# Kernel optimization log

Hardware: AMD Instinct MI355X
Metric: run time of the kernel (lower is better)

The kernel has to match this reference:

```python
import jax, jax.numpy as jnp
import numpy as np

B, S, T, D, H, FF = 4, 96, 96, 512, 8, 2048
DK = D // H
EPS = 1e-5
NEG_SLOPE = 0.01  # LeakyReLU default


def setup_inputs() -> dict:
    key = jax.random.key(0)
    ks = jax.random.split(key, 8)
    w = lambda k, shape: jax.random.normal(k, shape, jnp.float32) * 0.02
    return {
        "x": jax.random.normal(ks[0], (B, S, T, D), jnp.float32),
        "mask_bias": jax.random.uniform(ks[1], (B, S, T), jnp.float32),
        "t_w": w(ks[2], (4, D, D)), "t_b": jnp.zeros((4, D), jnp.float32),
        "s_w": w(ks[3], (4, D, D)), "s_b": jnp.zeros((4, D), jnp.float32),
        "fc_w1": w(ks[4], (D, FF)), "fc_b1": jnp.zeros((FF,), jnp.float32),
        "fc_w2": w(ks[5], (FF, D)), "fc_b2": jnp.zeros((D,), jnp.float32),
        "ln1_g": jnp.ones((D,), jnp.float32), "ln1_b": jnp.zeros((D,), jnp.float32),
        "ln2_g": jnp.ones((D,), jnp.float32), "ln2_b": jnp.zeros((D,), jnp.float32),
    }


def _ln(y, g, b):
    m = y.mean(-1, keepdims=True)
    v = ((y - m) ** 2).mean(-1, keepdims=True)
    return (y - m) / jnp.sqrt(v + EPS) * g + b


def _split_heads(y):
    # (B,S,T,D) -> (B,H,S,T,DK)
    b, s, t, _ = y.shape
    return y.reshape(b, s, t, H, DK).transpose(0, 3, 1, 2, 4)


def _mha(x, w, b, mask_bias, time_axis):
    q = _split_heads(x @ w[0] + b[0])
    k = _split_heads(x @ w[1] + b[1])
    v = _split_heads(x @ w[2] + b[2])
    scale = 1.0 / np.sqrt(DK)
    if time_axis:
        # attention over time axis T: scores (B,H,S,T,T)
        p = jax.nn.softmax(jnp.einsum('bhstd,bhsud->bhstu', q, k) * scale, axis=-1)
        p = p * mask_bias[:, None, :, :, None]            # post-softmax mask
        o = jnp.einsum('bhstu,bhsud->bhstd', p, v)
    else:
        # attention over space axis S: scores (B,H,T,S,S)
        p = jax.nn.softmax(jnp.einsum('bhstd,bhutd->bhtsu', q, k) * scale, axis=-1)
        p = p * mask_bias.transpose(0, 2, 1)[:, None, :, :, None]
        o = jnp.einsum('bhtsu,bhutd->bhstd', p, v)
    o = o.transpose(0, 2, 3, 1, 4).reshape(x.shape)
    return o @ w[3] + b[3]


def reference(x, mask_bias, t_w, t_b, s_w, s_b, fc_w1, fc_b1, fc_w2, fc_b2,
              ln1_g, ln1_b, ln2_g, ln2_b):
    tt = _mha(x, t_w, t_b, mask_bias, True)
    ss = _mha(tt, s_w, s_b, mask_bias, False)
    x1 = _ln(x + ss, ln1_g, ln1_b)
    h = x1 @ fc_w1 + fc_b1
    h = jnp.where(h >= 0, h, NEG_SLOPE * h)
    ff = h @ fc_w2 + fc_b2
    return _ln(x1 + ff, ln2_g, ln2_b)
```

## Files before the change

### kernel.cpp

```cpp
#include <hip/hip_runtime.h>
#include <hip/hip_bf16.h>

#define B_ 4
#define S_ 96
#define T_ 96
#define D_ 512
#define H_ 8
#define FF_ 2048
#define NROWS (B_*S_*T_)
#define EPS_ 1e-5f
#define NEG_ 0.01f
#define DD_ (512*512)

typedef unsigned short u16;
typedef __attribute__((ext_vector_type(8))) short bf16x8;
typedef __attribute__((ext_vector_type(4))) float f32x4;
typedef __attribute__((address_space(1))) const unsigned glb_u32;
typedef __attribute__((address_space(3))) unsigned lds_u32;

__device__ __forceinline__ float bf(u16 u) { return __uint_as_float(((unsigned)u) << 16); }
__device__ __forceinline__ u16 f2bf(float f) {
    __hip_bfloat16 h = __float2bfloat16(f);
    return *reinterpret_cast<u16*>(&h);
}
__device__ __forceinline__ float blo(unsigned v) { return __uint_as_float(v << 16); }
__device__ __forceinline__ float bhi(unsigned v) { return __uint_as_float(v & 0xffff0000u); }

__device__ __forceinline__ float cvt_ld(float x) { return x; }
__device__ __forceinline__ float cvt_ld(u16 x)  { return bf(x); }
__device__ __forceinline__ void cvt_st(float* p, float v) { *p = v; }
__device__ __forceinline__ void cvt_st(u16* p, float v)   { *p = f2bf(v); }

__device__ __forceinline__ void load8(const float* p, float* y) {
    float4 a = *(const float4*)p, b = *(const float4*)(p + 4);
    y[0]=a.x; y[1]=a.y; y[2]=a.z; y[3]=a.w; y[4]=b.x; y[5]=b.y; y[6]=b.z; y[7]=b.w;
}
__device__ __forceinline__ void load8(const u16* p, float* y) {
    uint4 u = *(const uint4*)p;
    y[0]=blo(u.x); y[1]=bhi(u.x); y[2]=blo(u.y); y[3]=bhi(u.y);
    y[4]=blo(u.z); y[5]=bhi(u.z); y[6]=blo(u.w); y[7]=bhi(u.w);
}
__device__ __forceinline__ void store8(float* p, const float* y) {
    *(float4*)p       = make_float4(y[0], y[1], y[2], y[3]);
    *(float4*)(p + 4) = make_float4(y[4], y[5], y[6], y[7]);
}
__device__ __forceinline__ void store8(u16* p, const float* y) {
    ushort4 a, b;
    a.x = f2bf(y[0]); a.y = f2bf(y[1]); a.z = f2bf(y[2]); a.w = f2bf(y[3]);
    b.x = f2bf(y[4]); b.y = f2bf(y[5]); b.z = f2bf(y[6]); b.w = f2bf(y[7]);
    *(ushort4*)p = a; *(ushort4*)(p + 4) = b;
}

__global__ __launch_bounds__(256)
void cvt_f32_bf16(const float* __restrict__ in, u16* __restrict__ out)
{
    const size_t i = ((size_t)blockIdx.x * 256 + threadIdx.x) * 8;
    float y[8];
    load8(in + i, y);
    store8(out + i, y);
}

__global__ __launch_bounds__(256)
void tconv(const float* __restrict__ in, u16* __restrict__ out, int R, int C)
{
    __shared__ float t[32][33];
    const int c0 = blockIdx.x * 32, r0 = blockIdx.y * 32;
    const int tr = threadIdx.x >> 3, c4 = (threadIdx.x & 7) * 4;
    float4 v = *(const float4*)(in + (size_t)(r0 + tr) * C + c0 + c4);
    t[tr][c4] = v.x; t[tr][c4 + 1] = v.y; t[tr][c4 + 2] = v.z; t[tr][c4 + 3] = v.w;
    __syncthreads();
    const int oc = tr, r4 = c4;
    ushort4 u;
    u.x = f2bf(t[r4 + 0][oc]); u.y = f2bf(t[r4 + 1][oc]);
    u.z = f2bf(t[r4 + 2][oc]); u.w = f2bf(t[r4 + 3][oc]);
    *(ushort4*)(out + (size_t)(c0 + oc) * R + r0 + r4) = u;
}

__global__ __launch_bounds__(256)
void tconv8(const float* __restrict__ t_w, const float* __restrict__ s_w,
            u16* __restrict__ out)
{
    __shared__ float t[32][33];
    const int z = blockIdx.z;
    const float* in = (z < 4) ? (t_w + (size_t)z * DD_) : (s_w + (size_t)(z - 4) * DD_);
    u16* o = out + (size_t)z * DD_;
    const int c0 = blockIdx.x * 32, r0 = blockIdx.y * 32;
    const int tr = threadIdx.x >> 3, c4 = (threadIdx.x & 7) * 4;
    float4 v = *(const float4*)(in + (size_t)(r0 + tr) * 512 + c0 + c4);
    t[tr][c4] = v.x; t[tr][c4 + 1] = v.y; t[tr][c4 + 2] = v.z; t[tr][c4 + 3] = v.w;
    __syncthreads();
    const int oc = tr, r4 = c4;
    ushort4 u;
    u.x = f2bf(t[r4 + 0][oc]); u.y = f2bf(t[r4 + 1][oc]);
    u.z = f2bf(t[r4 + 2][oc]); u.w = f2bf(t[r4 + 3][oc]);
    *(ushort4*)(o + (size_t)(c0 + oc) * 512 + r0 + r4) = u;
}

#define GEMM_PRE()                                                              \
    const int tid = threadIdx.x;                                                \
    const int w = tid >> 6, l = tid & 63;                                       \
    const int wr = w >> 1, wc = w & 1;                                          \
    const unsigned gx = gridDim.x;                                              \
    const unsigned nwg = gx * gridDim.y;                                        \
    unsigned f = blockIdx.y * gx + blockIdx.x;                                  \
    f = (f & 7) * (nwg >> 3) + (f >> 3);                                        \
    const int lrow = l >> 3;                                                    \
    const int swz8 = (((l & 7) ^ lrow) << 3);                                   \
    const int fr16 = l & 15;                                                    \
    const int kq = l >> 4;

#define GEMM_COMPUTE()                                                          \
    _Pragma("unroll")                                                           \
    for (int kk = 0; kk < 2; ++kk) {                                            \
        const int sw = ((((kk << 2) | kq)) ^ (fr16 & 7)) << 3;                  \
        bf16x8 af[4], bfr[4];                                                   \
        _Pragma("unroll")                                                       \
        for (int i = 0; i < 4; ++i)                                             \
            af[i] = *(bf16x8*)&As[(wr * 64 + i * 16 + fr16) * 64 + sw];         \
        _Pragma("unroll")                                                       \
        for (int j = 0; j < 4; ++j)                                             \
            bfr[j] = *(bf16x8*)&Bs[(wc * 64 + j * 16 + fr16) * 64 + sw];        \
        _Pragma("unroll")                                                       \
        for (int i = 0; i < 4; ++i)                                             \
            _Pragma("unroll")                                                   \
            for (int j = 0; j < 4; ++j)                                         \
                acc[i][j] = __builtin_amdgcn_mfma_f32_16x16x32_bf16(af[i], bfr[j], acc[i][j], 0, 0, 0); \
    }

template<int ACT, bool ACC, typename TC>
__global__ __launch_bounds__(256)
void gemm2(const u16* __restrict__ A, const u16* __restrict__ WT,
           const float* __restrict__ bias, TC* __restrict__ C,
           int K, int lda, int ldwt, int ldc)
{
    __shared__ u16 As[128 * 64];
    __shared__ u16 Bs[128 * 64];
    GEMM_PRE();
    const int row0 = (int)(f / gx) * 128, col0 = (int)(f % gx) * 128;
    f32x4 acc[4][4] = {};

    for (int kt = 0; kt < K; kt += 64) {
#pragma unroll
        for (int j = 0; j < 4; ++j) {
            const int line = w * 32 + j * 8;
            const u16* asrc = A  + (size_t)(row0 + line + lrow) * lda  + kt + swz8;
            const u16* bsrc = WT + (size_t)(col0 + line + lrow) * ldwt + kt + swz8;
            __builtin_amdgcn_global_load_lds((glb_u32*)asrc, (lds_u32*)&As[line * 64], 16, 0, 0);
            __builtin_amdgcn_global_load_lds((glb_u32*)bsrc, (lds_u32*)&Bs[line * 64], 16, 0, 0);
        }
        __syncthreads();
        GEMM_COMPUTE();
        __syncthreads();
    }
    const int crow = kq * 4;
#pragma unroll
    for (int i = 0; i < 4; ++i)
#pragma unroll
        for (int j = 0; j < 4; ++j) {
            const int col = col0 + wc * 64 + j * 16 + fr16;
            const float bv = ACC ? 0.f : bias[col];
#pragma unroll
            for (int e = 0; e < 4; ++e) {
                const size_t r = (size_t)(row0 + wr * 64 + i * 16 + crow + e);
                TC* cp = &C[r * (size_t)ldc + col];
                float v = acc[i][j][e] + bv;
                if (ACC) v += cvt_ld(*cp);
                if (ACT == 1) v = (v >= 0.f) ? v : NEG_ * v;
                cvt_st(cp, v);
            }
        }
}

template<int ACT, typename TC>
__global__ __launch_bounds__(512)
void gemm3(const u16* __restrict__ A, const u16* __restrict__ WT,
           const float* __restrict__ bias,
           TC* __restrict__ p0, TC* __restrict__ p1, TC* __restrict__ p2,
           int K, int lda, int ldwt, int ldc, int pgshift)
{
    __shared__ u16 lds[65536];
    const int tid = threadIdx.x;
    const int w = tid >> 6, l = tid & 63;
    const int wr = w >> 2, wc = w & 3;
    const unsigned gx = gridDim.x;
    const unsigned nwg = gx * gridDim.y;
    unsigned f = blockIdx.y * gx + blockIdx.x;
    f = (f & 7) * (nwg >> 3) + (f >> 3);
    const int row0 = (int)(f / gx) * 256, colg0 = (int)(f % gx) * 256;
    const int lrow = l >> 3;
    const int swz8 = (((l & 7) ^ lrow) << 3);
    const int fr16 = l & 15;
    const int kq = l >> 4;

    f32x4 acc[8][4] = {};
    const int NT = K >> 6;

    auto stage = [&](int buf, int kt) {
        u16* Ad = lds + buf * 16384;
        u16* Bd = lds + 32768 + buf * 16384;
#pragma unroll
        for (int j = 0; j < 4; ++j) {
            const int lineb = j * 64 + w * 8;
            const int srow = lineb + lrow;
            const u16* asrc = A  + (size_t)(row0  + srow) * lda  + kt + swz8;
            const u16* bsrc = WT + (size_t)(colg0 + srow) * ldwt + kt + swz8;
            __builtin_amdgcn_global_load_lds((glb_u32*)asrc, (lds_u32*)&Ad[lineb * 64], 16, 0, 0);
            __builtin_amdgcn_global_load_lds((glb_u32*)bsrc, (lds_u32*)&Bd[lineb * 64], 16, 0, 0);
        }
    };

    stage(0, 0);
    for (int t = 0; t < NT; ++t) {
        const int cur = t & 1;
        if (t + 1 < NT) {
            stage(cur ^ 1, (t + 1) << 6);
            asm volatile("s_waitcnt vmcnt(8)" ::: "memory");
        } else {
            asm volatile("s_waitcnt vmcnt(0)" ::: "memory");
        }
        __builtin_amdgcn_s_barrier();
        const u16* Ab = lds + cur * 16384;
        const u16* Bb = lds + 32768 + cur * 16384;
        bf16x8 bq[4];
#pragma unroll
        for (int p = 0; p < 4; ++p) {
            const int kk = p >> 1, ih = p & 1;
            const int sw = ((((kk << 2) | kq)) ^ (fr16 & 7)) << 3;
            if (ih == 0) {
#pragma unroll
                for (int j = 0; j < 4; ++j)
                    bq[j] = *(bf16x8*)&Bb[(wc * 64 + j * 16 + fr16) * 64 + sw];
            }
            bf16x8 af[4];
#pragma unroll
            for (int i = 0; i < 4; ++i)
                af[i] = *(bf16x8*)&Ab[(wr * 128 + (ih * 4 + i) * 16 + fr16) * 64 + sw];
            __builtin_amdgcn_s_barrier();
            __builtin_amdgcn_s_setprio(1);
#pragma unroll
            for (int i = 0; i < 4; ++i)
#pragma unroll
                for (int j = 0; j < 4; ++j)
                    acc[ih * 4 + i][j] = __builtin_amdgcn_mfma_f32_16x16x32_bf16(
                        af[i], bq[j], acc[ih * 4 + i][j], 0, 0, 0);
            __builtin_amdgcn_s_setprio(0);
        }
    }
    const int crow = kq * 4;
#pragma unroll
    for (int i = 0; i < 8; ++i)
#pragma unroll
        for (int j = 0; j < 4; ++j) {
            const int colg = colg0 + wc * 64 + j * 16 + fr16;
            TC* Cb = (((unsigned)colg >> pgshift) == 0) ? p0
                   : (((unsigned)colg >> pgshift) == 1) ? p1 : p2;
            const int col = colg & ((1 << pgshift) - 1);
            const float bv = bias[colg];
#pragma unroll
            for (int e = 0; e < 4; ++e) {
                const size_t r = (size_t)(row0 + wr * 128 + i * 16 + crow + e);
                float v = acc[i][j][e] + bv;
                if (ACT == 1) v = (v >= 0.f) ? v : NEG_ * v;
                cvt_st(&Cb[r * (size_t)ldc + col], v);
            }
        }
}

__global__ __launch_bounds__(384)
void attn_mfma(const u16* __restrict__ q, const u16* __restrict__ kbuf,
               const u16* __restrict__ vbuf, const float* __restrict__ mask,
               u16* __restrict__ out, int time_axis)
{
    __shared__ __align__(16) u16 Ks[96][72];
    __shared__ __align__(16) u16 VT[64][104];
    __shared__ __align__(16) u16 Ps[96][104];
    const int g = blockIdx.x;
    const int h = g & 7;
    const int bs = g >> 3;
    const int b = bs / 96, st = bs % 96;
    const size_t base   = time_axis ? ((size_t)(b * 96 + st) * 96) : ((size_t)b * 9216 + st);
    const size_t stride = time_axis ? 1 : 96;
    const int tid = threadIdx.x;
    const int w = tid / 64, l = tid & 63;
    const int fr = l & 15, fk = (l >> 4) * 8;

    for (int task = tid; task < 96 * 8; task += 384) {
        const int r = task >> 3, c = task & 7;
        *(uint4*)&Ks[r][c * 8] =
            *(const uint4*)(kbuf + (base + (size_t)r * stride) * 512 + h * 64 + c * 8);
    }
    for (int task = tid; task < 96 * 8; task += 384) {
        const int r = task >> 3, c = task & 7;
        uint4 dv = *(const uint4*)(vbuf + (base + (size_t)r * stride) * 512 + h * 64 + c * 8);
        const u16* e = (const u16*)&dv;
#pragma unroll
        for (int j = 0; j < 8; ++j) VT[c * 8 + j][r] = e[j];
    }
    const u16* qp = q + (base + (size_t)(16 * w + fr) * stride) * 512 + h * 64;
    bf16x8 aq0 = *(const bf16x8*)(qp + fk);
    bf16x8 aq1 = *(const bf16x8*)(qp + 32 + fk);
    __syncthreads();

    f32x4 s[6] = {};
#pragma unroll
    for (int fc = 0; fc < 6; ++fc) {
        bf16x8 b0 = *(const bf16x8*)&Ks[fc * 16 + fr][fk];
        bf16x8 b1 = *(const bf16x8*)&Ks[fc * 16 + fr][32 + fk];
        s[fc] = __builtin_amdgcn_mfma_f32_16x16x32_bf16(aq0, b0, s[fc], 0, 0, 0);
        s[fc] = __builtin_amdgcn_mfma_f32_16x16x32_bf16(aq1, b1, s[fc], 0, 0, 0);
    }
    float mrow[4], lrow[4];
#pragma unroll
    for (int e = 0; e < 4; ++e) {
        float mx = s[0][e];
#pragma unroll
        for (int fc = 1; fc < 6; ++fc) mx = fmaxf(mx, s[fc][e]);
#pragma unroll
        for (int off = 1; off < 16; off <<= 1) mx = fmaxf(mx, __shfl_xor(mx, off));
        mrow[e] = mx * 0.125f;
        lrow[e] = 0.f;
    }
    const int e0 = (l >> 4) * 4;
#pragma unroll
    for (int fc = 0; fc < 6; ++fc) {
#pragma unroll
        for (int e = 0; e < 4; ++e) {
            const float p = __expf(fmaf(s[fc][e], 0.125f, -mrow[e]));
            lrow[e] += p;
            Ps[16 * w + e0 + e][fc * 16 + fr] = f2bf(p);
        }
    }
#pragma unroll
    for (int e = 0; e < 4; ++e)
#pragma unroll
        for (int off = 1; off < 16; off <<= 1) lrow[e] += __shfl_xor(lrow[e], off);

    __syncthreads();

    f32x4 oacc[4] = {};
#pragma unroll
    for (int ks = 0; ks < 3; ++ks) {
        bf16x8 ap = *(const bf16x8*)&Ps[16 * w + fr][ks * 32 + fk];
#pragma unroll
        for (int j = 0; j < 4; ++j) {
            bf16x8 bv = *(const bf16x8*)&VT[j * 16 + fr][ks * 32 + fk];
            oacc[j] = __builtin_amdgcn_mfma_f32_16x16x32_bf16(ap, bv, oacc[j], 0, 0, 0);
        }
    }
    float mk[4];
#pragma unroll
    for (int e = 0; e < 4; ++e) {
        const size_t qrow = base + (size_t)(16 * w + e0 + e) * stride;
        mk[e] = mask[qrow] / lrow[e];
    }
#pragma unroll
    for (int j = 0; j < 4; ++j)
#pragma unroll
        for (int e = 0; e < 4; ++e) {
            const size_t qrow = base + (size_t)(16 * w + e0 + e) * stride;
            out[qrow * 512 + h * 64 + j * 16 + fr] = f2bf(oacc[j][e] * mk[e]);
        }
}

template<typename TA, typename TB, typename TO>
__global__ __launch_bounds__(64)
void add_ln(const TA* __restrict__ a, const TB* __restrict__ bsrc,
            const float* __restrict__ g, const float* __restrict__ beta,
            TO* __restrict__ out)
{
    const size_t row = blockIdx.x;
    const int lane = threadIdx.x;
    float ya[8], yb[8], y[8];
    load8(a + row * D_ + lane * 8, ya);
    load8(bsrc + row * D_ + lane * 8, yb);
    float sum = 0.f, sq = 0.f;
#pragma unroll
    for (int i = 0; i < 8; ++i) { y[i] = ya[i] + yb[i]; sum += y[i]; sq += y[i] * y[i]; }
#pragma unroll
    for (int off = 32; off >= 1; off >>= 1) {
        sum += __shfl_xor(sum, off);
        sq  += __shfl_xor(sq, off);
    }
    const float mean = sum * (1.f / D_);
    const float var  = sq * (1.f / D_) - mean * mean;
    const float rstd = rsqrtf(var + EPS_);
    const float* gp = g + lane * 8;
    const float* bp = beta + lane * 8;
    float o[8];
#pragma unroll
    for (int i = 0; i < 8; ++i) o[i] = (y[i] - mean) * rstd * gp[i] + bp[i];
    store8(out + row * D_ + lane * 8, o);
}

extern "C" void kernel_launch(void* const* d_in, const int* in_sizes, int n_in,
                              void* d_out, int out_size, void* d_ws, size_t ws_size,
                              hipStream_t stream)
{
    const float* x     = (const float*)d_in[0];
    const float* mask  = (const float*)d_in[1];
    const float* t_w   = (const float*)d_in[2];
    const float* t_b   = (const float*)d_in[3];
    const float* s_w   = (const float*)d_in[4];
    const float* s_b   = (const float*)d_in[5];
    const float* fc_w1 = (const float*)d_in[6];
    const float* fc_b1 = (const float*)d_in[7];
    const float* fc_w2 = (const float*)d_in[8];
    const float* fc_b2 = (const float*)d_in[9];
    const float* ln1_g = (const float*)d_in[10];
    const float* ln1_b = (const float*)d_in[11];
    const float* ln2_g = (const float*)d_in[12];
    const float* ln2_b = (const float*)d_in[13];

    const size_t PG = (size_t)NROWS * 512;
    const size_t WTC = (size_t)2048 * 512 * 2;
    if (ws_size < (PG * 3 + WTC) * sizeof(u16)) return;
    u16* O0   = (u16*)d_out;
    u16* O1   = O0 + PG;
    u16* WS0  = (u16*)d_ws;
    u16* WS1  = WS0 + PG;
    u16* WS2  = WS1 + PG;
    u16* TAIL = WS0 + 3 * PG;

    const dim3 gblk(256);
    const dim3 g512(4, NROWS / 128);
    const dim3 qkv3grid(6, NROWS / 256);
    const dim3 h3grid(4, NROWS / 256);

    cvt_f32_bf16<<<dim3((unsigned)(PG / 2048)), gblk, 0, stream>>>(x, WS2);
    tconv8<<<dim3(16, 16, 8), gblk, 0, stream>>>(t_w, s_w, TAIL);
    gemm3<0, u16><<<qkv3grid, dim3(512), 0, stream>>>(
        WS2, TAIL, t_b, O0, WS0, WS1, 512, 512, 512, 512, 9);
    attn_mfma<<<dim3(B_ * H_ * 96), dim3(384), 0, stream>>>(O0, WS0, WS1, mask, O0, 1);
    gemm2<0, false, u16><<<g512, gblk, 0, stream>>>(
        O0, TAIL + (size_t)3 * DD_, t_b + 3 * 512, O1, 512, 512, 512, 512);
    gemm3<0, u16><<<qkv3grid, dim3(512), 0, stream>>>(
        O1, TAIL + (size_t)4 * DD_, s_b, O0, WS0, WS1, 512, 512, 512, 512, 9);
    attn_mfma<<<dim3(B_ * H_ * 96), dim3(384), 0, stream>>>(O0, WS0, WS1, mask, O0, 0);
    gemm2<0, false, u16><<<g512, gblk, 0, stream>>>(
        O0, TAIL + (size_t)7 * DD_, s_b + 3 * 512, O1, 512, 512, 512, 512);
    add_ln<u16, u16, u16><<<dim3(NROWS), dim3(64), 0, stream>>>(WS2, O1, ln1_g, ln1_b, WS2);
    u16* WT1f = TAIL;
    u16* WT2f = TAIL + (size_t)2048 * 512;
    tconv<<<dim3(64, 16), gblk, 0, stream>>>(fc_w1, WT1f, 512, 2048);
    tconv<<<dim3(16, 64), gblk, 0, stream>>>(fc_w2, WT2f, 2048, 512);
    gemm3<1, u16><<<h3grid, dim3(512), 0, stream>>>(
        WS2, WT1f, fc_b1, O0, O0, O0, 512, 512, 512, 1024, 30);
    gemm2<0, false, u16><<<g512, gblk, 0, stream>>>(O0, WT2f, fc_b2, WS1, 1024, 1024, 2048, 512);
    gemm3<1, u16><<<h3grid, dim3(512), 0, stream>>>(
        WS2, WT1f + (size_t)1024 * 512, fc_b1 + 1024, O0, O0, O0, 512, 512, 512, 1024, 30);
    gemm2<0, true, u16><<<g512, gblk, 0, stream>>>(O0, WT2f + 1024, nullptr, WS1, 1024, 1024, 2048, 512);
    add_ln<u16, u16, float><<<dim3(NROWS), dim3(64), 0, stream>>>(
        WS2, WS1, ln2_g, ln2_b, (float*)d_out);
}
```

Before: 568.5 us.

## Fold temporal output projection into spatial QKV weights and restructure FFN chunking

```diff
diff --git a/kernel.cpp b/kernel.cpp
--- a/kernel.cpp
+++ b/kernel.cpp
@@ -87,6 +87,12 @@
     const int c0 = blockIdx.x * 32, r0 = blockIdx.y * 32;
     const int tr = threadIdx.x >> 3, c4 = (threadIdx.x & 7) * 4;
     float4 v = *(const float4*)(in + (size_t)(r0 + tr) * 512 + c0 + c4);
+    if (z == 3) {
+        ushort4 u;
+        u.x = f2bf(v.x); u.y = f2bf(v.y); u.z = f2bf(v.z); u.w = f2bf(v.w);
+        *(ushort4*)(o + (size_t)(r0 + tr) * 512 + c0 + c4) = u;
+        return;
+    }
     t[tr][c4] = v.x; t[tr][c4 + 1] = v.y; t[tr][c4 + 2] = v.z; t[tr][c4 + 3] = v.w;
     __syncthreads();
     const int oc = tr, r4 = c4;
@@ -94,6 +100,23 @@
     u.x = f2bf(t[r4 + 0][oc]); u.y = f2bf(t[r4 + 1][oc]);
     u.z = f2bf(t[r4 + 2][oc]); u.w = f2bf(t[r4 + 3][oc]);
     *(ushort4*)(o + (size_t)(c0 + oc) * 512 + r0 + r4) = u;
+}
+
+__global__ __launch_bounds__(256)
+void fbias_k(const u16* __restrict__ WTs, const float* __restrict__ tb3,
+             const float* __restrict__ sb, float* __restrict__ fb)
+{
+    const int j = blockIdx.x * 256 + threadIdx.x;
+    const u16* row = WTs + (size_t)j * 512;
+    float acc = sb[j];
+    for (int k = 0; k < 512; k += 8) {
+        float y[8], t[8];
+        load8(row + k, y);
+        load8(tb3 + k, t);
+        acc += y[0]*t[0] + y[1]*t[1] + y[2]*t[2] + y[3]*t[3]
+             + y[4]*t[4] + y[5]*t[5] + y[6]*t[6] + y[7]*t[7];
+    }
+    fb[j] = acc;
 }
 
 #define GEMM_PRE()                                                              \
@@ -158,7 +181,7 @@
 #pragma unroll
         for (int j = 0; j < 4; ++j) {
             const int col = col0 + wc * 64 + j * 16 + fr16;
-            const float bv = ACC ? 0.f : bias[col];
+            const float bv = (ACC || ACT == 2) ? 0.f : bias[col];
 #pragma unroll
             for (int e = 0; e < 4; ++e) {
                 const size_t r = (size_t)(row0 + wr * 64 + i * 16 + crow + e);
@@ -424,18 +447,20 @@
     const dim3 gblk(256);
     const dim3 g512(4, NROWS / 128);
     const dim3 qkv3grid(6, NROWS / 256);
-    const dim3 h3grid(4, NROWS / 256);
+    const dim3 h3grid(8, 72);
 
     cvt_f32_bf16<<<dim3((unsigned)(PG / 2048)), gblk, 0, stream>>>(x, WS2);
     tconv8<<<dim3(16, 16, 8), gblk, 0, stream>>>(t_w, s_w, TAIL);
     gemm3<0, u16><<<qkv3grid, dim3(512), 0, stream>>>(
         WS2, TAIL, t_b, O0, WS0, WS1, 512, 512, 512, 512, 9);
+    gemm2<2, false, u16><<<dim3(4, 12), gblk, 0, stream>>>(
+        TAIL + (size_t)4 * DD_, TAIL + (size_t)3 * DD_, nullptr, TAIL, 512, 512, 512, 512);
+    float* fb = (float*)(TAIL + (size_t)3 * DD_);
+    fbias_k<<<dim3(6), gblk, 0, stream>>>(TAIL + (size_t)4 * DD_, t_b + 3 * 512, s_b, fb);
     attn_mfma<<<dim3(B_ * H_ * 96), dim3(384), 0, stream>>>(O0, WS0, WS1, mask, O0, 1);
-    gemm2<0, false, u16><<<g512, gblk, 0, stream>>>(
-        O0, TAIL + (size_t)3 * DD_, t_b + 3 * 512, O1, 512, 512, 512, 512);
     gemm3<0, u16><<<qkv3grid, dim3(512), 0, stream>>>(
-        O1, TAIL + (size_t)4 * DD_, s_b, O0, WS0, WS1, 512, 512, 512, 512, 9);
-    attn_mfma<<<dim3(B_ * H_ * 96), dim3(384), 0, stream>>>(O0, WS0, WS1, mask, O0, 0);
+        O0, TAIL, fb, O1, WS0, WS1, 512, 512, 512, 512, 9);
+    attn_mfma<<<dim3(B_ * H_ * 96), dim3(384), 0, stream>>>(O1, WS0, WS1, mask, O0, 0);
     gemm2<0, false, u16><<<g512, gblk, 0, stream>>>(
         O0, TAIL + (size_t)7 * DD_, s_b + 3 * 512, O1, 512, 512, 512, 512);
     add_ln<u16, u16, u16><<<dim3(NROWS), dim3(64), 0, stream>>>(WS2, O1, ln1_g, ln1_b, WS2);
@@ -443,12 +468,13 @@
     u16* WT2f = TAIL + (size_t)2048 * 512;
     tconv<<<dim3(64, 16), gblk, 0, stream>>>(fc_w1, WT1f, 512, 2048);
     tconv<<<dim3(16, 64), gblk, 0, stream>>>(fc_w2, WT2f, 2048, 512);
-    gemm3<1, u16><<<h3grid, dim3(512), 0, stream>>>(
-        WS2, WT1f, fc_b1, O0, O0, O0, 512, 512, 512, 1024, 30);
-    gemm2<0, false, u16><<<g512, gblk, 0, stream>>>(O0, WT2f, fc_b2, WS1, 1024, 1024, 2048, 512);
-    gemm3<1, u16><<<h3grid, dim3(512), 0, stream>>>(
-        WS2, WT1f + (size_t)1024 * 512, fc_b1 + 1024, O0, O0, O0, 512, 512, 512, 1024, 30);
-    gemm2<0, true, u16><<<g512, gblk, 0, stream>>>(O0, WT2f + 1024, nullptr, WS1, 1024, 1024, 2048, 512);
+    for (int r = 0; r < 2; ++r) {
+        const size_t off = (size_t)r * 18432;
+        gemm3<1, u16><<<h3grid, dim3(512), 0, stream>>>(
+            WS2 + off * 512, WT1f, fc_b1, O0, O0, O0, 512, 512, 512, 2048, 30);
+        gemm2<0, false, u16><<<dim3(4, 144), gblk, 0, stream>>>(
+            O0, WT2f, fc_b2, WS1 + off * 512, 2048, 2048, 2048, 512);
+    }
     add_ln<u16, u16, float><<<dim3(NROWS), dim3(64), 0, stream>>>(
         WS2, WS1, ln2_g, ln2_b, (float*)d_out);
 }
```

Result: faster. 553.4 us (-2.7%).
